# Kernel tuning notes

Measured on AMD Instinct MI355X. Metric: run time of the kernel, lower is better.

Reference implementation:

```python
import jax, jax.numpy as jnp
import numpy as np

EMA_DECAY = 0.99
EPS = 1e-5
KSZ = 4096
D = 512

def setup_inputs() -> dict:
    key = jax.random.key(0)
    k1, k2 = jax.random.split(key)
    f_ipm = jax.random.normal(k1, (8, 4096, D), dtype=jnp.float32)
    K = jax.random.normal(k2, (KSZ, D), dtype=jnp.float32)
    ema_cluster_size = jnp.zeros((KSZ,), dtype=jnp.float32)
    ema_w = K  # buffer initialized as K.clone() in the torch module
    return {"f_ipm": f_ipm, "K": K, "ema_cluster_size": ema_cluster_size, "ema_w": ema_w}

def _cdist_sq(x, y):
    # squared euclidean pairwise distances [N, M]; argmin over these equals
    # argmin over torch.cdist (sqrt is monotonic)
    x2 = jnp.sum(x * x, axis=-1, keepdims=True)
    y2 = jnp.sum(y * y, axis=-1)
    return jnp.maximum(x2 + y2[None, :] - 2.0 * (x @ y.T), 0.0)

def reference(f_ipm, K, ema_cluster_size, ema_w):
    # Training-mode forward of IPLM with EMA codebook update (functional).
    B, T, d = f_ipm.shape
    Ksz = K.shape[0]
    f = f_ipm.reshape(-1, d)                     # [N, D]
    d2 = _cdist_sq(f, K)                         # [N, Ksz]
    k1_idx = jnp.argmin(d2, axis=1)              # [N]
    k1 = K[k1_idx]                               # [N, D] gather
    loss_lk = jnp.mean((jax.lax.stop_gradient(k1) - f) ** 2)
    # EMA cluster statistics via segment_sum (equivalent to one_hot.T @ f)
    counts = jax.ops.segment_sum(jnp.ones((f.shape[0],), f.dtype), k1_idx, num_segments=Ksz)
    dw = jax.ops.segment_sum(f, k1_idx, num_segments=Ksz)
    new_ecs = ema_cluster_size * EMA_DECAY + (1.0 - EMA_DECAY) * counts
    n = new_ecs.sum()
    smoothed = (new_ecs + EPS) / (n + Ksz * EPS) * n
    new_ema_w = ema_w * EMA_DECAY + (1.0 - EMA_DECAY) * dw
    new_K = new_ema_w / smoothed[:, None]
    f_ipmlm = k1.reshape(B, T, d)
    return (f_ipmlm, loss_lk, new_K, new_ecs, new_ema_w)
```

## Files before the change

kernel.cpp:

```cpp
#include <hip/hip_runtime.h>
#include <hip/hip_bf16.h>

#define NROWS 32768
#define DDIM  512
#define KSZ_  4096
#define EMA_DECAY_ 0.99f
#define EPS_ 1e-5f

#define BM 128
#define BN 128
#define NCHUNK 4
#define CSPLIT 8
#define BKB 64

typedef float f32x4 __attribute__((ext_vector_type(4)));
typedef __bf16 bf16x8 __attribute__((ext_vector_type(8)));

__device__ __forceinline__ void g2lds16(const __bf16* g, __bf16* l) {
    __builtin_amdgcn_global_load_lds(
        (const __attribute__((address_space(1))) void*)g,
        (__attribute__((address_space(3))) void*)l, 16, 0, 0);
}

__device__ __forceinline__ void cvt8(const float4 x0, const float4 x1,
                                     bf16x8& h, bf16x8& l) {
    float xs[8] = {x0.x, x0.y, x0.z, x0.w, x1.x, x1.y, x1.z, x1.w};
#pragma unroll
    for (int j = 0; j < 8; j++) {
        __bf16 hj = (__bf16)xs[j];
        h[j] = hj;
        l[j] = (__bf16)(xs[j] - (float)hj);
    }
}

__global__ __launch_bounds__(256) void convert_kernel(
    const float* __restrict__ src,
    __bf16* __restrict__ hi, __bf16* __restrict__ lo) {
    int g  = blockIdx.x * 256 + threadIdx.x;
    int s  = g & 7;
    int r  = (g >> 3) & 127;
    int ks = (g >> 10) & 7;
    int rb = g >> 13;
    int srck = ks * 64 + ((s ^ (r & 7)) * 8);
    const float* p = src + (size_t)(rb * 128 + r) * DDIM + srck;
    float4 x0 = *(const float4*)p;
    float4 x1 = *(const float4*)(p + 4);
    bf16x8 h, l;
    cvt8(x0, x1, h, l);
    *(bf16x8*)(hi + (size_t)g * 8) = h;
    *(bf16x8*)(lo + (size_t)g * 8) = l;
}

__global__ __launch_bounds__(256) void kt2_kernel(const float* __restrict__ K,
                                                  float* __restrict__ Kt2) {
    int gid  = blockIdx.x * 256 + threadIdx.x;
    int row  = gid >> 6;
    int lane = threadIdx.x & 63;
    const float* kr = K + (size_t)row * DDIM;
    float s = 0.f;
#pragma unroll
    for (int u = 0; u < 2; u++) {
        float4 v = *(const float4*)&kr[u * 256 + lane * 4];
        s += v.x * v.x + v.y * v.y + v.z * v.z + v.w * v.w;
    }
#pragma unroll
    for (int off = 1; off < 64; off <<= 1) s += __shfl_xor(s, off, 64);
    if (lane == 0) Kt2[row] = s;
}

__global__ __launch_bounds__(256, 2) void argmin_kernel(
    const __bf16* __restrict__ fh, const __bf16* __restrict__ fl,
    const __bf16* __restrict__ kh, const __bf16* __restrict__ kl,
    const float* __restrict__ Kt2,
    float* __restrict__ bestd, int* __restrict__ bestidx) {

    __shared__ __align__(16) __bf16 Ah[BM * BKB];
    __shared__ __align__(16) __bf16 Al[BM * BKB];
    __shared__ __align__(16) __bf16 Bh[BN * BKB];
    __shared__ __align__(16) __bf16 Bl[BN * BKB];
    __shared__ float redD[2][BM];
    __shared__ int   redI[2][BM];

    const int tid  = threadIdx.x;
    const int lane = tid & 63;
    const int w    = tid >> 6;
    const int wr   = w >> 1;
    const int wc   = w & 1;
    const int l15  = lane & 15;
    const int l4   = lane >> 4;
    const int rb   = blockIdx.x;
    const int split = blockIdx.y;

    float best[16];
    int   bidx[16];
#pragma unroll
    for (int i = 0; i < 16; i++) { best[i] = 3.4e38f; bidx[i] = 0x7fffffff; }

    for (int chunk = 0; chunk < NCHUNK; ++chunk) {
        const int cb = split * NCHUNK + chunk;
        const int c0 = cb * BN;
        f32x4 acc[4][4];
#pragma unroll
        for (int m = 0; m < 4; m++)
#pragma unroll
            for (int n = 0; n < 4; n++)
                acc[m][n] = (f32x4){0.f, 0.f, 0.f, 0.f};

        for (int ks = 0; ks < DDIM / BKB; ++ks) {
            const __bf16* tAh = fh + (size_t)(rb * 8 + ks) * (BM * BKB);
            const __bf16* tAl = fl + (size_t)(rb * 8 + ks) * (BM * BKB);
            const __bf16* tBh = kh + (size_t)(cb * 8 + ks) * (BN * BKB);
            const __bf16* tBl = kl + (size_t)(cb * 8 + ks) * (BN * BKB);
            __syncthreads();
#pragma unroll
            for (int i = 0; i < 4; i++) {
                const int gg  = i * 256 + tid;
                const int ub  = (i * 256 + w * 64) * 8;
                g2lds16(tAh + (size_t)gg * 8, Ah + ub);
                g2lds16(tAl + (size_t)gg * 8, Al + ub);
                g2lds16(tBh + (size_t)gg * 8, Bh + ub);
                g2lds16(tBl + (size_t)gg * 8, Bl + ub);
            }
            __syncthreads();

#pragma unroll
            for (int h = 0; h < 2; ++h) {
                bf16x8 av[4], alv[4], bv[4], blv[4];
#pragma unroll
                for (int m = 0; m < 4; m++) {
                    int row  = wr * 64 + m * 16 + l15;
                    int slot = (h * 4 + l4) ^ (l15 & 7);
                    int off  = row * BKB + slot * 8;
                    av[m]  = *(const bf16x8*)&Ah[off];
                    alv[m] = *(const bf16x8*)&Al[off];
                }
#pragma unroll
                for (int n = 0; n < 4; n++) {
                    int row  = wc * 64 + n * 16 + l15;
                    int slot = (h * 4 + l4) ^ (l15 & 7);
                    int off  = row * BKB + slot * 8;
                    bv[n]  = *(const bf16x8*)&Bh[off];
                    blv[n] = *(const bf16x8*)&Bl[off];
                }
#pragma unroll
                for (int m = 0; m < 4; m++)
#pragma unroll
                    for (int n = 0; n < 4; n++)
                        acc[m][n] = __builtin_amdgcn_mfma_f32_16x16x32_bf16(av[m], bv[n], acc[m][n], 0, 0, 0);
#pragma unroll
                for (int m = 0; m < 4; m++)
#pragma unroll
                    for (int n = 0; n < 4; n++)
                        acc[m][n] = __builtin_amdgcn_mfma_f32_16x16x32_bf16(av[m], blv[n], acc[m][n], 0, 0, 0);
#pragma unroll
                for (int m = 0; m < 4; m++)
#pragma unroll
                    for (int n = 0; n < 4; n++)
                        acc[m][n] = __builtin_amdgcn_mfma_f32_16x16x32_bf16(alv[m], bv[n], acc[m][n], 0, 0, 0);
            }
        }

        float kt2c[4];
#pragma unroll
        for (int n = 0; n < 4; n++) kt2c[n] = Kt2[c0 + wc * 64 + n * 16 + l15];
#pragma unroll
        for (int m = 0; m < 4; m++)
#pragma unroll
            for (int q = 0; q < 4; q++) {
                float d = 3.4e38f; int bi = 0x7fffffff;
#pragma unroll
                for (int n = 0; n < 4; n++) {
                    float s = 0.5f * kt2c[n] - acc[m][n][q];
                    int col = c0 + wc * 64 + n * 16 + l15;
                    if (s < d || (s == d && col < bi)) { d = s; bi = col; }
                }
                int i16 = m * 4 + q;
                if (d < best[i16] || (d == best[i16] && bi < bidx[i16])) {
                    best[i16] = d; bidx[i16] = bi;
                }
            }
    }

#pragma unroll
    for (int i = 0; i < 16; i++) {
        float d = best[i]; int bi = bidx[i];
#pragma unroll
        for (int off = 1; off < 16; off <<= 1) {
            float od = __shfl_xor(d, off, 64);
            int   oi = __shfl_xor(bi, off, 64);
            if (od < d || (od == d && oi < bi)) { d = od; bi = oi; }
        }
        if (l15 == 0) {
            int m = i >> 2, q = i & 3;
            int rl = wr * 64 + m * 16 + l4 * 4 + q;
            redD[wc][rl] = d;
            redI[wc][rl] = bi;
        }
    }
    __syncthreads();
    if (tid < BM) {
        float d0 = redD[0][tid], d1 = redD[1][tid];
        int   i0 = redI[0][tid], i1 = redI[1][tid];
        if (d1 < d0 || (d1 == d0 && i1 < i0)) { d0 = d1; i0 = i1; }
        bestd[(size_t)(rb * BM + tid) * CSPLIT + split]   = d0;
        bestidx[(size_t)(rb * BM + tid) * CSPLIT + split] = i0;
    }
}

__global__ __launch_bounds__(256) void reduce_kernel(
    const float* __restrict__ bestd, const int* __restrict__ bestidx,
    int* __restrict__ k1, int* __restrict__ cnt) {
    int row = blockIdx.x * 256 + threadIdx.x;
    float4 d0 = *(const float4*)&bestd[(size_t)row * CSPLIT];
    float4 d1 = *(const float4*)&bestd[(size_t)row * CSPLIT + 4];
    int4   i0 = *(const int4*)&bestidx[(size_t)row * CSPLIT];
    int4   i1 = *(const int4*)&bestidx[(size_t)row * CSPLIT + 4];
    float ds[8] = {d0.x, d0.y, d0.z, d0.w, d1.x, d1.y, d1.z, d1.w};
    int   is[8] = {i0.x, i0.y, i0.z, i0.w, i1.x, i1.y, i1.z, i1.w};
    float d = ds[0]; int bi = is[0];
#pragma unroll
    for (int s = 1; s < 8; s++)
        if (ds[s] < d || (ds[s] == d && is[s] < bi)) { d = ds[s]; bi = is[s]; }
    k1[row] = bi;
    atomicAdd(&cnt[bi], 1);
}

__global__ __launch_bounds__(256) void scan_ecs_kernel(
    const int* __restrict__ cnt, const float* __restrict__ ecs_in,
    int* __restrict__ offs, float* __restrict__ out_ecs,
    float* __restrict__ n_sum) {
    __shared__ int sums[256];
    __shared__ float fs[256];
    int t = threadIdx.x;
    int local[16];
    int s = 0;
    float fsum = 0.f;
#pragma unroll
    for (int i = 0; i < 16; i++) { local[i] = cnt[t * 16 + i]; s += local[i]; }
    sums[t] = s;
#pragma unroll
    for (int i = 0; i < 16; i++) {
        float v = ecs_in[t * 16 + i] * EMA_DECAY_
                + (1.0f - EMA_DECAY_) * (float)local[i];
        out_ecs[t * 16 + i] = v;
        fsum += v;
    }
    fs[t] = fsum;
    __syncthreads();
    for (int off = 1; off < 256; off <<= 1) {
        int v = (t >= off) ? sums[t - off] : 0;
        __syncthreads();
        sums[t] += v;
        __syncthreads();
    }
    int run = sums[t] - s;
#pragma unroll
    for (int i = 0; i < 16; i++) { offs[t * 16 + i] = run; run += local[i]; }
    for (int off = 128; off > 0; off >>= 1) {
        if (t < off) fs[t] += fs[t + off];
        __syncthreads();
    }
    if (t == 0) *n_sum = fs[0];
}

__global__ __launch_bounds__(256) void scatter_kernel(
    const int* __restrict__ k1, const int* __restrict__ offs,
    int* __restrict__ cursor, int* __restrict__ bucket) {
    int row = blockIdx.x * 256 + threadIdx.x;
    int bi = k1[row];
    int pos = atomicAdd(&cursor[bi], 1);
    bucket[offs[bi] + pos] = row;
}

__global__ __launch_bounds__(256) void gather_kernel(
    const float* __restrict__ f, const float* __restrict__ K,
    const int* __restrict__ k1,
    float* __restrict__ out_fipm, float* __restrict__ loss_sum) {
    __shared__ float ls[4];
    int tid  = threadIdx.x;
    int wid  = (blockIdx.x * 256 + tid) >> 6;
    int lane = tid & 63;
    float lsum = 0.f;
#pragma unroll
    for (int rr = 0; rr < 8; rr++) {
        int row = wid * 8 + rr;
        int bi  = k1[row];
        const float* frow = f + (size_t)row * DDIM;
        const float* krow = K + (size_t)bi * DDIM;
#pragma unroll
        for (int u = 0; u < 2; u++) {
            int off = u * 256 + lane * 4;
            float4 fv = *(const float4*)&frow[off];
            float4 kv = *(const float4*)&krow[off];
            *(float4*)&out_fipm[(size_t)row * DDIM + off] = kv;
            float dx = kv.x - fv.x, dy = kv.y - fv.y;
            float dz = kv.z - fv.z, dwv = kv.w - fv.w;
            lsum += dx * dx + dy * dy + dz * dz + dwv * dwv;
        }
    }
#pragma unroll
    for (int off = 1; off < 64; off <<= 1) lsum += __shfl_xor(lsum, off, 64);
    if (lane == 0) ls[tid >> 6] = lsum;
    __syncthreads();
    if (tid == 0) atomicAdd(loss_sum, ls[0] + ls[1] + ls[2] + ls[3]);
}

__global__ __launch_bounds__(256) void dwfinal_kernel(
    const float* __restrict__ f, const float* __restrict__ ema_w,
    const int* __restrict__ offs, const int* __restrict__ cnt,
    const int* __restrict__ bucket,
    const float* __restrict__ out_ecs, const float* __restrict__ n_sum,
    const float* __restrict__ loss_sum,
    float* __restrict__ out_K, float* __restrict__ out_emaw,
    float* __restrict__ out_loss) {
    int j = blockIdx.x;
    int t = threadIdx.x;
    int beg = offs[j];
    int c   = cnt[j];
    float2 acc = {0.f, 0.f};
    int i = 0;
    for (; i + 1 < c; i += 2) {
        int r0 = bucket[beg + i];
        int r1 = bucket[beg + i + 1];
        float2 a = *(const float2*)&f[(size_t)r0 * DDIM + t * 2];
        float2 b = *(const float2*)&f[(size_t)r1 * DDIM + t * 2];
        acc.x += a.x + b.x;
        acc.y += a.y + b.y;
    }
    if (i < c) {
        int r0 = bucket[beg + i];
        float2 a = *(const float2*)&f[(size_t)r0 * DDIM + t * 2];
        acc.x += a.x;
        acc.y += a.y;
    }
    float n = *n_sum;
    float smoothed = (out_ecs[j] + EPS_) / (n + KSZ_ * EPS_) * n;
    float inv = 1.0f / smoothed;
    float2 wv = *(const float2*)&ema_w[(size_t)j * DDIM + t * 2];
    float w0 = EMA_DECAY_ * wv.x + (1.0f - EMA_DECAY_) * acc.x;
    float w1 = EMA_DECAY_ * wv.y + (1.0f - EMA_DECAY_) * acc.y;
    size_t e = (size_t)j * DDIM + t * 2;
    out_emaw[e + 0] = w0; out_emaw[e + 1] = w1;
    out_K[e + 0] = w0 * inv; out_K[e + 1] = w1 * inv;
    if (j == 0 && t == 0) *out_loss = *loss_sum * (1.0f / 16777216.0f);
}

extern "C" void kernel_launch(void* const* d_in, const int* in_sizes, int n_in,
                              void* d_out, int out_size, void* d_ws, size_t ws_size,
                              hipStream_t stream) {
    const float* f     = (const float*)d_in[0];
    const float* K     = (const float*)d_in[1];
    const float* ecs   = (const float*)d_in[2];
    const float* ema_w = (const float*)d_in[3];

    float* ws       = (float*)d_ws;
    float* Kt2      = ws;
    float* bestd    = ws + 4096;
    int*   bestidx  = (int*)(ws + 266240);
    float* loss_sum = ws + 528384;
    float* n_sum    = ws + 528385;
    int*   cnt      = (int*)(ws + 528386);
    int*   cursor   = (int*)(ws + 532482);
    int*   offs     = (int*)(ws + 536578);
    int*   k1       = (int*)(ws + 540674);
    int*   bucket   = (int*)(ws + 573442);
    __bf16* fh      = (__bf16*)(ws + 606212);
    __bf16* fl      = (__bf16*)(ws + 8994820);
    __bf16* kh      = (__bf16*)(ws + 17383428);
    __bf16* kl      = (__bf16*)(ws + 18432004);

    float* out      = (float*)d_out;
    float* out_fipm = out;
    float* out_loss = out + 16777216;
    float* out_K    = out + 16777217;
    float* out_ecs  = out + 18874369;
    float* out_emaw = out + 18878465;

    hipMemsetAsync(loss_sum, 0, (size_t)(2 + 4096 + 4096) * sizeof(float), stream);

    convert_kernel<<<NROWS * DDIM / 8 / 256, 256, 0, stream>>>(f, fh, fl);
    convert_kernel<<<KSZ_ * DDIM / 8 / 256, 256, 0, stream>>>(K, kh, kl);

    kt2_kernel<<<KSZ_ * 64 / 256, 256, 0, stream>>>(K, Kt2);

    dim3 grid(NROWS / BM, CSPLIT);
    argmin_kernel<<<grid, 256, 0, stream>>>(fh, fl, kh, kl, Kt2, bestd, bestidx);

    reduce_kernel<<<NROWS / 256, 256, 0, stream>>>(bestd, bestidx, k1, cnt);
    scan_ecs_kernel<<<1, 256, 0, stream>>>(cnt, ecs, offs, out_ecs, n_sum);
    scatter_kernel<<<NROWS / 256, 256, 0, stream>>>(k1, offs, cursor, bucket);

    gather_kernel<<<NROWS / 8 / 4, 256, 0, stream>>>(f, K, k1, out_fipm, loss_sum);

    dwfinal_kernel<<<KSZ_, 256, 0, stream>>>(
        f, ema_w, offs, cnt, bucket, out_ecs, n_sum, loss_sum,
        out_K, out_emaw, out_loss);
}
```

Before: 715.0 us.

## Load A operand fragments directly from global in MFMA layout, bypassing LDS

Result: no change. 718.5 us (+0.5%).

```diff
diff --git a/kernel.cpp b/kernel.cpp
--- a/kernel.cpp
+++ b/kernel.cpp
@@ -33,7 +33,28 @@
     }
 }
 
-__global__ __launch_bounds__(256) void convert_kernel(
+__global__ __launch_bounds__(256) void convert_f_kernel(
+    const float* __restrict__ src,
+    __bf16* __restrict__ hi, __bf16* __restrict__ lo) {
+    int g   = blockIdx.x * 256 + threadIdx.x;
+    int l15 = g & 15;
+    int l4  = (g >> 4) & 3;
+    int khf = (g >> 6) & 1;
+    int g16 = (g >> 7) & 7;
+    int ks  = (g >> 10) & 7;
+    int rb  = g >> 13;
+    int row = rb * 128 + g16 * 16 + l15;
+    int k   = ks * 64 + (khf * 4 + l4) * 8;
+    const float* p = src + (size_t)row * DDIM + k;
+    float4 x0 = *(const float4*)p;
+    float4 x1 = *(const float4*)(p + 4);
+    bf16x8 h, l;
+    cvt8(x0, x1, h, l);
+    *(bf16x8*)(hi + (size_t)g * 8) = h;
+    *(bf16x8*)(lo + (size_t)g * 8) = l;
+}
+
+__global__ __launch_bounds__(256) void convert_k_kernel(
     const float* __restrict__ src,
     __bf16* __restrict__ hi, __bf16* __restrict__ lo) {
     int g  = blockIdx.x * 256 + threadIdx.x;
@@ -69,13 +90,11 @@
 }
 
 __global__ __launch_bounds__(256, 2) void argmin_kernel(
-    const __bf16* __restrict__ fh, const __bf16* __restrict__ fl,
+    const __bf16* __restrict__ fhf, const __bf16* __restrict__ flf,
     const __bf16* __restrict__ kh, const __bf16* __restrict__ kl,
     const float* __restrict__ Kt2,
     float* __restrict__ bestd, int* __restrict__ bestidx) {
 
-    __shared__ __align__(16) __bf16 Ah[BM * BKB];
-    __shared__ __align__(16) __bf16 Al[BM * BKB];
     __shared__ __align__(16) __bf16 Bh[BN * BKB];
     __shared__ __align__(16) __bf16 Bl[BN * BKB];
     __shared__ float redD[2][BM];
@@ -107,8 +126,6 @@
                 acc[m][n] = (f32x4){0.f, 0.f, 0.f, 0.f};
 
         for (int ks = 0; ks < DDIM / BKB; ++ks) {
-            const __bf16* tAh = fh + (size_t)(rb * 8 + ks) * (BM * BKB);
-            const __bf16* tAl = fl + (size_t)(rb * 8 + ks) * (BM * BKB);
             const __bf16* tBh = kh + (size_t)(cb * 8 + ks) * (BN * BKB);
             const __bf16* tBl = kl + (size_t)(cb * 8 + ks) * (BN * BKB);
             __syncthreads();
@@ -116,24 +133,24 @@
             for (int i = 0; i < 4; i++) {
                 const int gg  = i * 256 + tid;
                 const int ub  = (i * 256 + w * 64) * 8;
-                g2lds16(tAh + (size_t)gg * 8, Ah + ub);
-                g2lds16(tAl + (size_t)gg * 8, Al + ub);
                 g2lds16(tBh + (size_t)gg * 8, Bh + ub);
                 g2lds16(tBl + (size_t)gg * 8, Bl + ub);
             }
+            bf16x8 av[2][4], alv[2][4];
+#pragma unroll
+            for (int khf = 0; khf < 2; ++khf)
+#pragma unroll
+                for (int m = 0; m < 4; m++) {
+                    size_t e = ((size_t)(((rb * 8 + ks) * 8 + (wr * 4 + m)) * 2
+                                + khf)) * 512 + lane * 8;
+                    av[khf][m]  = *(const bf16x8*)&fhf[e];
+                    alv[khf][m] = *(const bf16x8*)&flf[e];
+                }
             __syncthreads();
 
 #pragma unroll
             for (int h = 0; h < 2; ++h) {
-                bf16x8 av[4], alv[4], bv[4], blv[4];
-#pragma unroll
-                for (int m = 0; m < 4; m++) {
-                    int row  = wr * 64 + m * 16 + l15;
-                    int slot = (h * 4 + l4) ^ (l15 & 7);
-                    int off  = row * BKB + slot * 8;
-                    av[m]  = *(const bf16x8*)&Ah[off];
-                    alv[m] = *(const bf16x8*)&Al[off];
-                }
+                bf16x8 bv[4], blv[4];
 #pragma unroll
                 for (int n = 0; n < 4; n++) {
                     int row  = wc * 64 + n * 16 + l15;
@@ -146,17 +163,17 @@
                 for (int m = 0; m < 4; m++)
 #pragma unroll
                     for (int n = 0; n < 4; n++)
-                        acc[m][n] = __builtin_amdgcn_mfma_f32_16x16x32_bf16(av[m], bv[n], acc[m][n], 0, 0, 0);
+                        acc[m][n] = __builtin_amdgcn_mfma_f32_16x16x32_bf16(av[h][m], bv[n], acc[m][n], 0, 0, 0);
 #pragma unroll
                 for (int m = 0; m < 4; m++)
 #pragma unroll
                     for (int n = 0; n < 4; n++)
-                        acc[m][n] = __builtin_amdgcn_mfma_f32_16x16x32_bf16(av[m], blv[n], acc[m][n], 0, 0, 0);
+                        acc[m][n] = __builtin_amdgcn_mfma_f32_16x16x32_bf16(av[h][m], blv[n], acc[m][n], 0, 0, 0);
 #pragma unroll
                 for (int m = 0; m < 4; m++)
 #pragma unroll
                     for (int n = 0; n < 4; n++)
-                        acc[m][n] = __builtin_amdgcn_mfma_f32_16x16x32_bf16(alv[m], bv[n], acc[m][n], 0, 0, 0);
+                        acc[m][n] = __builtin_amdgcn_mfma_f32_16x16x32_bf16(alv[h][m], bv[n], acc[m][n], 0, 0, 0);
             }
         }
 
@@ -282,8 +299,8 @@
     int lane = tid & 63;
     float lsum = 0.f;
 #pragma unroll
-    for (int rr = 0; rr < 8; rr++) {
-        int row = wid * 8 + rr;
+    for (int rr = 0; rr < 4; rr++) {
+        int row = wid * 4 + rr;
         int bi  = k1[row];
         const float* frow = f + (size_t)row * DDIM;
         const float* krow = K + (size_t)bi * DDIM;
@@ -364,8 +381,8 @@
     int*   offs     = (int*)(ws + 536578);
     int*   k1       = (int*)(ws + 540674);
     int*   bucket   = (int*)(ws + 573442);
-    __bf16* fh      = (__bf16*)(ws + 606212);
-    __bf16* fl      = (__bf16*)(ws + 8994820);
+    __bf16* fhf     = (__bf16*)(ws + 606212);
+    __bf16* flf     = (__bf16*)(ws + 8994820);
     __bf16* kh      = (__bf16*)(ws + 17383428);
     __bf16* kl      = (__bf16*)(ws + 18432004);
 
@@ -378,19 +395,19 @@
 
     hipMemsetAsync(loss_sum, 0, (size_t)(2 + 4096 + 4096) * sizeof(float), stream);
 
-    convert_kernel<<<NROWS * DDIM / 8 / 256, 256, 0, stream>>>(f, fh, fl);
-    convert_kernel<<<KSZ_ * DDIM / 8 / 256, 256, 0, stream>>>(K, kh, kl);
+    convert_f_kernel<<<NROWS * DDIM / 8 / 256, 256, 0, stream>>>(f, fhf, flf);
+    convert_k_kernel<<<KSZ_ * DDIM / 8 / 256, 256, 0, stream>>>(K, kh, kl);
 
     kt2_kernel<<<KSZ_ * 64 / 256, 256, 0, stream>>>(K, Kt2);
 
     dim3 grid(NROWS / BM, CSPLIT);
-    argmin_kernel<<<grid, 256, 0, stream>>>(fh, fl, kh, kl, Kt2, bestd, bestidx);
+    argmin_kernel<<<grid, 256, 0, stream>>>(fhf, flf, kh, kl, Kt2, bestd, bestidx);
 
     reduce_kernel<<<NROWS / 256, 256, 0, stream>>>(bestd, bestidx, k1, cnt);
     scan_ecs_kernel<<<1, 256, 0, stream>>>(cnt, ecs, offs, out_ecs, n_sum);
     scatter_kernel<<<NROWS / 256, 256, 0, stream>>>(k1, offs, cursor, bucket);
 
-    gather_kernel<<<NROWS / 8 / 4, 256, 0, stream>>>(f, K, k1, out_fipm, loss_sum);
+    gather_kernel<<<NROWS / 16, 256, 0, stream>>>(f, K, k1, out_fipm, loss_sum);
 
     dwfinal_kernel<<<KSZ_, 256, 0, stream>>>(
         f, ema_w, offs, cnt, bucket, out_ecs, n_sum, loss_sum,
```
